# Kernel tuning notes

Measured on AMD Instinct MI355X. Metric: run time of the kernel, lower is better.

Reference implementation:

```python
import jax, jax.numpy as jnp
import numpy as np


def _fq(x, scale, qmin, qmax):
    """Symmetric per-tensor fake-quant with straight-through rounding."""
    q = jnp.clip(jnp.round(x / scale), qmin, qmax) * scale
    return x + jax.lax.stop_gradient(q - x)


def _quant_weight(W):
    # Int8WeightPerTensorFloat: symmetric, narrow range [-127, 127],
    # scale = max|W| / 127 (per tensor).
    scale = jnp.max(jnp.abs(W)) / 127.0
    return _fq(W, scale, -127.0, 127.0)


def setup_inputs() -> dict:
    key = jax.random.key(0)
    ks = jax.random.split(key, 5)
    B, S, D, H = 64, 196, 768, 3072
    x = jax.random.normal(ks[0], (B, S, D), dtype=jnp.float32)
    W1 = jax.random.normal(ks[1], (H, D), dtype=jnp.float32) * (D ** -0.5)
    b1 = jax.random.normal(ks[2], (H,), dtype=jnp.float32) * 0.01
    W2 = jax.random.normal(ks[3], (D, H), dtype=jnp.float32) * (H ** -0.5)
    b2 = jax.random.normal(ks[4], (D,), dtype=jnp.float32) * 0.01
    # Learned activation quant scales (Int8ActPerTensorFloat params).
    s_gelu = jnp.float32(0.05)
    s_out = jnp.float32(0.02)
    return {"x": x, "W1": W1, "b1": b1, "W2": W2, "b2": b2,
            "s_gelu": s_gelu, "s_out": s_out}


def reference(x, W1, b1, W2, b2, s_gelu, s_out):
    # fc1 with int8 per-tensor fake-quantized weight (bias unquantized)
    h = jnp.einsum('bsd,hd->bsh', x, _quant_weight(W1)) + b1
    # GELU (exact, matching nn.GELU default) then int8 act fake-quant
    h = jax.nn.gelu(h, approximate=False)
    h = _fq(h, s_gelu, -128.0, 127.0)
    # fc2 with quantized weight, then output act fake-quant
    y = jnp.einsum('bsh,dh->bsd', h, _quant_weight(W2)) + b2
    y = _fq(y, s_out, -128.0, 127.0)
    return y
```

## Files before the change

### kernel.cpp

```cpp
#include <hip/hip_runtime.h>
#include <math.h>

typedef __attribute__((ext_vector_type(4))) int i32x4;
typedef __attribute__((ext_vector_type(4))) unsigned short u16x4;

#define MFMA_I8(a, b, c) __builtin_amdgcn_mfma_i32_16x16x64_i8((a), (b), (c), 0, 0, 0)

__device__ __forceinline__ void gload16(const void* g, void* l) {
    __builtin_amdgcn_global_load_lds(
        (const __attribute__((address_space(1))) unsigned int*)g,
        (__attribute__((address_space(3))) unsigned int*)l, 16, 0, 0);
}

__global__ void init_slots(unsigned* slots) {
    if (threadIdx.x < 3) slots[threadIdx.x] = 0u;
}

__global__ void absmax3_kernel(const float* __restrict__ W1, const float* __restrict__ W2,
                               const float* __restrict__ x, int n4w, int n4x,
                               unsigned* __restrict__ slots) {
    const float* p = (blockIdx.y == 0) ? W1 : (blockIdx.y == 1) ? W2 : x;
    const int n4 = (blockIdx.y == 2) ? n4x : n4w;
    float m = 0.f;
    const float4* p4 = (const float4*)p;
    for (int i = blockIdx.x * blockDim.x + threadIdx.x; i < n4; i += gridDim.x * blockDim.x) {
        float4 v = p4[i];
        m = fmaxf(m, fmaxf(fmaxf(fabsf(v.x), fabsf(v.y)), fmaxf(fabsf(v.z), fabsf(v.w))));
    }
#pragma unroll
    for (int off = 32; off > 0; off >>= 1)
        m = fmaxf(m, __shfl_xor(m, off, 64));
    if ((threadIdx.x & 63) == 0) atomicMax(slots + blockIdx.y, __float_as_uint(m));
}

__device__ __forceinline__ int pack4(float a, float b, float c, float d) {
    return (int)(((unsigned)(unsigned char)(signed char)(int)a) |
                 (((unsigned)(unsigned char)(signed char)(int)b) << 8) |
                 (((unsigned)(unsigned char)(signed char)(int)c) << 16) |
                 (((unsigned)(unsigned char)(signed char)(int)d) << 24));
}

__global__ void prep_kernel(const float* __restrict__ W1, signed char* __restrict__ o1,
                            const float* __restrict__ W2, signed char* __restrict__ o2,
                            const float* __restrict__ x, signed char* __restrict__ xq,
                            int n4w, int n4x, const unsigned* __restrict__ slots) {
    if (blockIdx.y < 2) {
        const float* W = blockIdx.y ? W2 : W1;
        signed char* out = blockIdx.y ? o2 : o1;
        const float inv_s = 127.0f / __uint_as_float(slots[blockIdx.y]);
        const float4* W4 = (const float4*)W;
        for (int i = blockIdx.x * blockDim.x + threadIdx.x; i < n4w; i += gridDim.x * blockDim.x) {
            float4 v = W4[i];
            float q0 = fminf(fmaxf(rintf(v.x * inv_s), -127.f), 127.f);
            float q1 = fminf(fmaxf(rintf(v.y * inv_s), -127.f), 127.f);
            float q2 = fminf(fmaxf(rintf(v.z * inv_s), -127.f), 127.f);
            float q3 = fminf(fmaxf(rintf(v.w * inv_s), -127.f), 127.f);
            *(int*)(out + 4 * (size_t)i) = pack4(q0, q1, q2, q3);
        }
    } else {
        const float sx = __uint_as_float(slots[2]) / 127.0f;
        const float inv_sx = 1.0f / sx;
        const float r_scale = 255.0f * inv_sx;
        const float4* x4 = (const float4*)x;
        for (int i = blockIdx.x * blockDim.x + threadIdx.x; i < n4x; i += gridDim.x * blockDim.x) {
            int r = i / 192;
            int c = (i - r * 192) * 4;
            float4 v = x4[i];
            float a0 = rintf(v.x * inv_sx), a1 = rintf(v.y * inv_sx);
            float a2 = rintf(v.z * inv_sx), a3 = rintf(v.w * inv_sx);
            float b0 = fminf(fmaxf(rintf((v.x - sx * a0) * r_scale), -127.f), 127.f);
            float b1 = fminf(fmaxf(rintf((v.y - sx * a1) * r_scale), -127.f), 127.f);
            float b2 = fminf(fmaxf(rintf((v.z - sx * a2) * r_scale), -127.f), 127.f);
            float b3 = fminf(fmaxf(rintf((v.w - sx * a3) * r_scale), -127.f), 127.f);
            size_t base = (size_t)r * 1536 + c;
            *(int*)(xq + base) = pack4(a0, a1, a2, a3);
            *(int*)(xq + base + 768) = pack4(b0, b1, b2, b3);
        }
    }
}

template <int EPI>
__global__ __launch_bounds__(512, 2) void gemm_i8(
    const signed char* __restrict__ A, const signed char* __restrict__ B,
    const float* __restrict__ bias, const unsigned* __restrict__ slots,
    const float* __restrict__ sg_ptr, const float* __restrict__ so_ptr,
    signed char* __restrict__ out_b, float* __restrict__ out_f,
    int N, int lda, int ldb, int NT, int bwrap, int fold_t) {
    extern __shared__ char smem[];

    const int tid = threadIdx.x;
    const int lane = tid & 63;
    const int w = tid >> 6;
    const int wm = (w >> 2) * 128;
    const int wn = (w & 3) * 64;
    const int lr16 = lane & 15;
    const int lkg = lane >> 4;

    const int gX = gridDim.x;
    const int nwg = gX * gridDim.y;
    const int orig = blockIdx.y * gX + blockIdx.x;
    const int qq = nwg >> 3, rr = nwg & 7;
    const int xcd = orig & 7, idx = orig >> 3;
    const int wg = (xcd < rr ? xcd * (qq + 1) : rr * (qq + 1) + (xcd - rr) * qq) + idx;
    const int m0 = (wg % gX) * 256;
    const int n0 = (wg / gX) * 256;

    const int rAb = (wm + lr16) * 128;
    const int rBb = (wn + lr16) * 128;
    const int lxor = lane & 7;
    const int c0 = (lkg ^ lxor) * 16;
    const int c1 = ((4 + lkg) ^ lxor) * 16;

    const int rsub = lane >> 3;
    const int csw = ((lane & 7) ^ rsub) * 16;

    const signed char* aSrc[2][2];
    const signed char* bSrc[2][2];
#pragma unroll
    for (int h = 0; h < 2; ++h)
#pragma unroll
        for (int L = 0; L < 2; ++L) {
            aSrc[h][L] = A + (size_t)(m0 + h * 128 + (w * 2 + L) * 8 + rsub) * lda + csw;
            bSrc[h][L] = B + (size_t)(n0 + h * 128 + (w * 2 + L) * 8 + rsub) * ldb + csw;
        }
    const int ldsCh = w * 2048;

#define STAGE_A(P, KC)                                 \
    do {                                               \
        char* _d = smem + ((P) << 15) + ldsCh;         \
        gload16(aSrc[0][0] + (KC), _d);                \
        gload16(aSrc[0][1] + (KC), _d + 1024);         \
        gload16(aSrc[1][0] + (KC), _d + 16384);        \
        gload16(aSrc[1][1] + (KC), _d + 17408);        \
    } while (0)
#define STAGE_B(P, KC)                                 \
    do {                                               \
        char* _d = smem + 65536 + ((P) << 15) + ldsCh; \
        gload16(bSrc[0][0] + (KC), _d);                \
        gload16(bSrc[0][1] + (KC), _d + 1024);         \
        gload16(bSrc[1][0] + (KC), _d + 16384);        \
        gload16(bSrc[1][1] + (KC), _d + 17408);        \
    } while (0)

    i32x4 acc[8][4] = {};
    i32x4 a[4][2], b[4][2];

    STAGE_A(0, 0);
    STAGE_B(0, 0);
    STAGE_A(1, 128);
    STAGE_B(1, 128);
    asm volatile("s_waitcnt vmcnt(8)" ::: "memory");
    __builtin_amdgcn_s_barrier();

    for (int t = 0; t < NT; ++t) {
        if (t == fold_t) {
#pragma unroll
            for (int mi = 0; mi < 8; ++mi)
#pragma unroll
                for (int ni = 0; ni < 4; ++ni)
                    acc[mi][ni] *= 255;
        }
        const int p = t & 1;
        const char* Ab = smem + (p << 15);
        const char* Bb = smem + 65536 + (p << 15);
        const bool pre = (t + 2) < NT;
        const int kc = (t + 2) << 7;
        const int bc = (kc >= bwrap) ? kc - bwrap : kc;

#pragma unroll
        for (int j = 0; j < 4; ++j) {
            a[j][0] = *(const i32x4*)(Ab + rAb + j * 2048 + c0);
            a[j][1] = *(const i32x4*)(Ab + rAb + j * 2048 + c1);
        }
#pragma unroll
        for (int n = 0; n < 4; ++n) {
            b[n][0] = *(const i32x4*)(Bb + rBb + n * 2048 + c0);
            b[n][1] = *(const i32x4*)(Bb + rBb + n * 2048 + c1);
        }
        __builtin_amdgcn_s_setprio(1);
#pragma unroll
        for (int kk = 0; kk < 2; ++kk)
#pragma unroll
            for (int j = 0; j < 4; ++j)
#pragma unroll
                for (int n = 0; n < 4; ++n)
                    acc[j][n] = MFMA_I8(a[j][kk], b[n][kk], acc[j][n]);
        __builtin_amdgcn_s_setprio(0);
        __builtin_amdgcn_s_barrier();
        if (pre) STAGE_B(p, bc);

#pragma unroll
        for (int j = 0; j < 4; ++j) {
            a[j][0] = *(const i32x4*)(Ab + rAb + (4 + j) * 2048 + c0);
            a[j][1] = *(const i32x4*)(Ab + rAb + (4 + j) * 2048 + c1);
        }
        __builtin_amdgcn_s_setprio(1);
#pragma unroll
        for (int kk = 0; kk < 2; ++kk)
#pragma unroll
            for (int j = 0; j < 4; ++j)
#pragma unroll
                for (int n = 0; n < 2; ++n)
                    acc[4 + j][n] = MFMA_I8(a[j][kk], b[n][kk], acc[4 + j][n]);
        __builtin_amdgcn_s_setprio(0);
        __builtin_amdgcn_s_barrier();
        if (pre) STAGE_A(p, kc);

        __builtin_amdgcn_s_setprio(1);
#pragma unroll
        for (int kk = 0; kk < 2; ++kk)
#pragma unroll
            for (int j = 0; j < 4; ++j)
#pragma unroll
                for (int n = 2; n < 4; ++n)
                    acc[4 + j][n] = MFMA_I8(a[j][kk], b[n][kk], acc[4 + j][n]);
        __builtin_amdgcn_s_setprio(0);
        if (pre) {
            asm volatile("s_waitcnt vmcnt(8)" ::: "memory");
        } else {
            asm volatile("s_waitcnt vmcnt(0)" ::: "memory");
        }
        __builtin_amdgcn_s_barrier();
    }

    const float s1 = __uint_as_float(slots[EPI]) / 127.0f;
    const int mbase = m0 + wm + lkg * 4;
    const int nbase = n0 + wn + lr16;
    if constexpr (EPI == 0) {
        const float sx = __uint_as_float(slots[2]) / 127.0f;
        const float c1s = sx * s1 * (1.0f / 255.0f);
        const float inv_sg = 1.0f / *sg_ptr;
#pragma unroll
        for (int mi = 0; mi < 8; ++mi)
#pragma unroll
            for (int ni = 0; ni < 4; ++ni) {
                const int n = nbase + ni * 16;
                const float bn = bias[n];
#pragma unroll
                for (int e = 0; e < 4; ++e) {
                    const int m = mbase + mi * 16 + e;
                    float h = (float)acc[mi][ni][e] * c1s + bn;
                    float g = 0.5f * h * (1.0f + erff(h * 0.70710678118654752f));
                    float q = fminf(fmaxf(rintf(g * inv_sg), -128.f), 127.f);
                    out_b[(size_t)m * N + n] = (signed char)(int)q;
                }
            }
    } else {
        const float sg = *sg_ptr;
        const float so = *so_ptr;
        const float inv_so = 1.0f / so;
        const float c2s = sg * s1;
#pragma unroll
        for (int mi = 0; mi < 8; ++mi)
#pragma unroll
            for (int ni = 0; ni < 4; ++ni) {
                const int n = nbase + ni * 16;
                const float bn = bias[n];
#pragma unroll
                for (int e = 0; e < 4; ++e) {
                    const int m = mbase + mi * 16 + e;
                    float y = (float)acc[mi][ni][e] * c2s + bn;
                    float q = fminf(fmaxf(rintf(y * inv_so), -128.f), 127.f);
                    out_f[(size_t)m * N + n] = q * so;
                }
            }
    }
#undef STAGE_A
#undef STAGE_B
}

extern "C" void kernel_launch(void* const* d_in, const int* in_sizes, int n_in,
                              void* d_out, int out_size, void* d_ws, size_t ws_size,
                              hipStream_t stream) {
    const float* x  = (const float*)d_in[0];
    const float* W1 = (const float*)d_in[1];
    const float* b1 = (const float*)d_in[2];
    const float* W2 = (const float*)d_in[3];
    const float* b2 = (const float*)d_in[4];
    const float* sg = (const float*)d_in[5];
    const float* so = (const float*)d_in[6];

    const int M = 64 * 196;
    const int D = 768;
    const int H = 3072;

    char* ws = (char*)d_ws;
    unsigned* slots = (unsigned*)ws;
    signed char* xq    = (signed char*)(ws + 256);
    signed char* w1int = xq + (size_t)M * 1536;
    signed char* w2int = w1int + (size_t)H * D;
    signed char* qact  = w2int + (size_t)D * H;

    hipFuncSetAttribute(reinterpret_cast<const void*>(gemm_i8<0>),
                        hipFuncAttributeMaxDynamicSharedMemorySize, 131072);
    hipFuncSetAttribute(reinterpret_cast<const void*>(gemm_i8<1>),
                        hipFuncAttributeMaxDynamicSharedMemorySize, 131072);

    init_slots<<<1, 64, 0, stream>>>(slots);
    const int n4w = (H * D) / 4;
    const int n4x = (M * D) / 4;
    absmax3_kernel<<<dim3(512, 3), 256, 0, stream>>>(W1, W2, x, n4w, n4x, slots);
    prep_kernel<<<dim3(1024, 3), 256, 0, stream>>>(W1, w1int, W2, w2int, x, xq,
                                                   n4w, n4x, slots);

    dim3 g1(M / 256, H / 256);
    gemm_i8<0><<<g1, 512, 131072, stream>>>(
        xq, w1int, b1, slots, sg, so, qact, nullptr, H, 1536, D, 12, D, 6);

    dim3 g2(M / 256, D / 256);
    gemm_i8<1><<<g2, 512, 131072, stream>>>(
        qact, w2int, b2, slots, sg, so, nullptr, (float*)d_out, D, H, H, 24, 1 << 30, -1);
}
```

Before: 265.8 us.

## Shrink GEMM tile to 256x128 with K=64 stages for higher occupancy

Retiles both int8 GEMMs from 256x256 block tiles with a K-step of 128 to 256x128 tiles with a K-step of 64. LDS drops from 128KB to 48KB per block and launch bounds rise to 4 blocks per SM. The LDS layout, swizzle and wave mapping are rewritten to fit. The aim is more resident waves and more blocks in flight to hide latency. The cost is lower arithmetic intensity per block, more global loads per FLOP, and twice as many loop iterations with barriers.

```diff
diff --git a/kernel.cpp b/kernel.cpp
--- a/kernel.cpp
+++ b/kernel.cpp
@@ -2,7 +2,6 @@
 #include <math.h>
 
 typedef __attribute__((ext_vector_type(4))) int i32x4;
-typedef __attribute__((ext_vector_type(4))) unsigned short u16x4;
 
 #define MFMA_I8(a, b, c) __builtin_amdgcn_mfma_i32_16x16x64_i8((a), (b), (c), 0, 0, 0)
 
@@ -80,7 +79,7 @@
 }
 
 template <int EPI>
-__global__ __launch_bounds__(512, 2) void gemm_i8(
+__global__ __launch_bounds__(512, 4) void gemm_i8(
     const signed char* __restrict__ A, const signed char* __restrict__ B,
     const float* __restrict__ bias, const unsigned* __restrict__ slots,
     const float* __restrict__ sg_ptr, const float* __restrict__ so_ptr,
@@ -91,8 +90,8 @@
     const int tid = threadIdx.x;
     const int lane = tid & 63;
     const int w = tid >> 6;
-    const int wm = (w >> 2) * 128;
-    const int wn = (w & 3) * 64;
+    const int wm = (w >> 1) * 64;
+    const int wn = (w & 1) * 64;
     const int lr16 = lane & 15;
     const int lkg = lane >> 4;
 
@@ -103,120 +102,93 @@
     const int xcd = orig & 7, idx = orig >> 3;
     const int wg = (xcd < rr ? xcd * (qq + 1) : rr * (qq + 1) + (xcd - rr) * qq) + idx;
     const int m0 = (wg % gX) * 256;
-    const int n0 = (wg / gX) * 256;
-
-    const int rAb = (wm + lr16) * 128;
-    const int rBb = (wn + lr16) * 128;
-    const int lxor = lane & 7;
-    const int c0 = (lkg ^ lxor) * 16;
-    const int c1 = ((4 + lkg) ^ lxor) * 16;
-
-    const int rsub = lane >> 3;
-    const int csw = ((lane & 7) ^ rsub) * 16;
-
-    const signed char* aSrc[2][2];
-    const signed char* bSrc[2][2];
-#pragma unroll
-    for (int h = 0; h < 2; ++h)
-#pragma unroll
-        for (int L = 0; L < 2; ++L) {
-            aSrc[h][L] = A + (size_t)(m0 + h * 128 + (w * 2 + L) * 8 + rsub) * lda + csw;
-            bSrc[h][L] = B + (size_t)(n0 + h * 128 + (w * 2 + L) * 8 + rsub) * ldb + csw;
-        }
-    const int ldsCh = w * 2048;
-
-#define STAGE_A(P, KC)                                 \
-    do {                                               \
-        char* _d = smem + ((P) << 15) + ldsCh;         \
-        gload16(aSrc[0][0] + (KC), _d);                \
-        gload16(aSrc[0][1] + (KC), _d + 1024);         \
-        gload16(aSrc[1][0] + (KC), _d + 16384);        \
-        gload16(aSrc[1][1] + (KC), _d + 17408);        \
+    const int n0 = (wg / gX) * 128;
+
+    const int h8 = lr16 >> 1;
+    const int pG = (((lr16 & 1) << 2) + lkg) ^ h8;
+    const int rdA = wm * 64 + h8 * 128 + pG * 16;
+    const int rdB = 32768 + wn * 64 + h8 * 128 + pG * 16;
+
+    const int Lw = lane >> 3;
+    const int ll = (lane & 7) ^ Lw;
+    const int dr = ll >> 2;
+    const int dk = (ll & 3) << 4;
+    const signed char* aSrc0 = A + (size_t)(m0 + w * 32 + 2 * Lw + dr) * lda + dk;
+    const signed char* aSrc1 = A + (size_t)(m0 + w * 32 + 16 + 2 * Lw + dr) * lda + dk;
+    const signed char* bSrc  = B + (size_t)(n0 + w * 16 + 2 * Lw + dr) * ldb + dk;
+
+#define STAGE_A(P, KC)                                  \
+    do {                                                \
+        char* _d = smem + ((P) << 14) + w * 2048;       \
+        gload16(aSrc0 + (KC), _d);                      \
+        gload16(aSrc1 + (KC), _d + 1024);               \
     } while (0)
-#define STAGE_B(P, KC)                                 \
-    do {                                               \
-        char* _d = smem + 65536 + ((P) << 15) + ldsCh; \
-        gload16(bSrc[0][0] + (KC), _d);                \
-        gload16(bSrc[0][1] + (KC), _d + 1024);         \
-        gload16(bSrc[1][0] + (KC), _d + 16384);        \
-        gload16(bSrc[1][1] + (KC), _d + 17408);        \
+#define STAGE_B(P, KC)                                  \
+    do {                                                \
+        char* _d = smem + 32768 + ((P) << 13) + w * 1024; \
+        gload16(bSrc + (KC), _d);                       \
     } while (0)
 
-    i32x4 acc[8][4] = {};
-    i32x4 a[4][2], b[4][2];
+    i32x4 acc[4][4] = {};
+    i32x4 a[4], b[4];
 
     STAGE_A(0, 0);
     STAGE_B(0, 0);
-    STAGE_A(1, 128);
-    STAGE_B(1, 128);
-    asm volatile("s_waitcnt vmcnt(8)" ::: "memory");
+    STAGE_A(1, 64);
+    STAGE_B(1, 64);
+    asm volatile("s_waitcnt vmcnt(3)" ::: "memory");
     __builtin_amdgcn_s_barrier();
 
     for (int t = 0; t < NT; ++t) {
         if (t == fold_t) {
 #pragma unroll
-            for (int mi = 0; mi < 8; ++mi)
+            for (int mi = 0; mi < 4; ++mi)
 #pragma unroll
                 for (int ni = 0; ni < 4; ++ni)
                     acc[mi][ni] *= 255;
         }
         const int p = t & 1;
-        const char* Ab = smem + (p << 15);
-        const char* Bb = smem + 65536 + (p << 15);
+        const char* Ab = smem + (p << 14);
+        const char* Bb = smem + (p << 13);
         const bool pre = (t + 2) < NT;
-        const int kc = (t + 2) << 7;
+        const int kc = (t + 2) << 6;
         const int bc = (kc >= bwrap) ? kc - bwrap : kc;
 
 #pragma unroll
-        for (int j = 0; j < 4; ++j) {
-            a[j][0] = *(const i32x4*)(Ab + rAb + j * 2048 + c0);
-            a[j][1] = *(const i32x4*)(Ab + rAb + j * 2048 + c1);
-        }
-#pragma unroll
-        for (int n = 0; n < 4; ++n) {
-            b[n][0] = *(const i32x4*)(Bb + rBb + n * 2048 + c0);
-            b[n][1] = *(const i32x4*)(Bb + rBb + n * 2048 + c1);
-        }
+        for (int f = 0; f < 2; ++f) a[f] = *(const i32x4*)(Ab + rdA + f * 1024);
+#pragma unroll
+        for (int n = 0; n < 4; ++n) b[n] = *(const i32x4*)(Bb + rdB + n * 1024);
         __builtin_amdgcn_s_setprio(1);
 #pragma unroll
-        for (int kk = 0; kk < 2; ++kk)
-#pragma unroll
-            for (int j = 0; j < 4; ++j)
-#pragma unroll
-                for (int n = 0; n < 4; ++n)
-                    acc[j][n] = MFMA_I8(a[j][kk], b[n][kk], acc[j][n]);
+        for (int f = 0; f < 2; ++f)
+#pragma unroll
+            for (int n = 0; n < 4; ++n)
+                acc[f][n] = MFMA_I8(a[f], b[n], acc[f][n]);
         __builtin_amdgcn_s_setprio(0);
         __builtin_amdgcn_s_barrier();
         if (pre) STAGE_B(p, bc);
 
 #pragma unroll
-        for (int j = 0; j < 4; ++j) {
-            a[j][0] = *(const i32x4*)(Ab + rAb + (4 + j) * 2048 + c0);
-            a[j][1] = *(const i32x4*)(Ab + rAb + (4 + j) * 2048 + c1);
-        }
+        for (int f = 2; f < 4; ++f) a[f] = *(const i32x4*)(Ab + rdA + f * 1024);
         __builtin_amdgcn_s_setprio(1);
 #pragma unroll
-        for (int kk = 0; kk < 2; ++kk)
-#pragma unroll
-            for (int j = 0; j < 4; ++j)
-#pragma unroll
-                for (int n = 0; n < 2; ++n)
-                    acc[4 + j][n] = MFMA_I8(a[j][kk], b[n][kk], acc[4 + j][n]);
+        for (int f = 2; f < 4; ++f)
+#pragma unroll
+            for (int n = 0; n < 2; ++n)
+                acc[f][n] = MFMA_I8(a[f], b[n], acc[f][n]);
         __builtin_amdgcn_s_setprio(0);
         __builtin_amdgcn_s_barrier();
         if (pre) STAGE_A(p, kc);
 
         __builtin_amdgcn_s_setprio(1);
 #pragma unroll
-        for (int kk = 0; kk < 2; ++kk)
-#pragma unroll
-            for (int j = 0; j < 4; ++j)
-#pragma unroll
-                for (int n = 2; n < 4; ++n)
-                    acc[4 + j][n] = MFMA_I8(a[j][kk], b[n][kk], acc[4 + j][n]);
+        for (int f = 2; f < 4; ++f)
+#pragma unroll
+            for (int n = 2; n < 4; ++n)
+                acc[f][n] = MFMA_I8(a[f], b[n], acc[f][n]);
         __builtin_amdgcn_s_setprio(0);
         if (pre) {
-            asm volatile("s_waitcnt vmcnt(8)" ::: "memory");
+            asm volatile("s_waitcnt vmcnt(3)" ::: "memory");
         } else {
             asm volatile("s_waitcnt vmcnt(0)" ::: "memory");
         }
@@ -231,7 +203,7 @@
         const float c1s = sx * s1 * (1.0f / 255.0f);
         const float inv_sg = 1.0f / *sg_ptr;
 #pragma unroll
-        for (int mi = 0; mi < 8; ++mi)
+        for (int mi = 0; mi < 4; ++mi)
 #pragma unroll
             for (int ni = 0; ni < 4; ++ni) {
                 const int n = nbase + ni * 16;
@@ -251,7 +223,7 @@
         const float inv_so = 1.0f / so;
         const float c2s = sg * s1;
 #pragma unroll
-        for (int mi = 0; mi < 8; ++mi)
+        for (int mi = 0; mi < 4; ++mi)
 #pragma unroll
             for (int ni = 0; ni < 4; ++ni) {
                 const int n = nbase + ni * 16;
@@ -292,9 +264,9 @@
     signed char* qact  = w2int + (size_t)D * H;
 
     hipFuncSetAttribute(reinterpret_cast<const void*>(gemm_i8<0>),
-                        hipFuncAttributeMaxDynamicSharedMemorySize, 131072);
+                        hipFuncAttributeMaxDynamicSharedMemorySize, 49152);
     hipFuncSetAttribute(reinterpret_cast<const void*>(gemm_i8<1>),
-                        hipFuncAttributeMaxDynamicSharedMemorySize, 131072);
+                        hipFuncAttributeMaxDynamicSharedMemorySize, 49152);
 
     init_slots<<<1, 64, 0, stream>>>(slots);
     const int n4w = (H * D) / 4;
@@ -303,11 +275,11 @@
     prep_kernel<<<dim3(1024, 3), 256, 0, stream>>>(W1, w1int, W2, w2int, x, xq,
                                                    n4w, n4x, slots);
 
-    dim3 g1(M / 256, H / 256);
-    gemm_i8<0><<<g1, 512, 131072, stream>>>(
-        xq, w1int, b1, slots, sg, so, qact, nullptr, H, 1536, D, 12, D, 6);
-
-    dim3 g2(M / 256, D / 256);
-    gemm_i8<1><<<g2, 512, 131072, stream>>>(
-        qact, w2int, b2, slots, sg, so, nullptr, (float*)d_out, D, H, H, 24, 1 << 30, -1);
-}
+    dim3 g1(M / 256, H / 128);
+    gemm_i8<0><<<g1, 512, 49152, stream>>>(
+        xq, w1int, b1, slots, sg, so, qact, nullptr, H, 1536, D, 24, D, 12);
+
+    dim3 g2(M / 256, D / 128);
+    gemm_i8<1><<<g2, 512, 49152, stream>>>(
+        qact, w2int, b2, slots, sg, so, nullptr, (float*)d_out, D, 3072, H, 48, 1 << 30, -1);
+}
```

Measured after the change: 253.5 us. 4.6% less time.
